# Kernel tuning notes

Measured on AMD Instinct MI355X. Metric: run time of the kernel, lower is better.

The kernel has to match this reference:

```python
import jax, jax.numpy as jnp
import numpy as np

B, T, D, H, E = 32, 512, 768, 12, 6  # batch, seq(=input_size), n_embd, num_heads, per-head dim
DFF = 4 * D
EPS = 1e-5


def setup_inputs() -> dict:
    key = jax.random.key(0)
    ks = jax.random.split(key, 10)
    s = 0.02
    return {
        "x": jax.random.normal(ks[0], (B, T, D), jnp.float32),
        "Wq": jax.random.normal(ks[1], (H, D, E), jnp.float32) * s,
        "Wk": jax.random.normal(ks[2], (H, D, E), jnp.float32) * s,
        "Wv": jax.random.normal(ks[3], (H, D, E), jnp.float32) * s,
        "Wo": jax.random.normal(ks[4], (H * E, D), jnp.float32) * s,
        "bo": jnp.zeros((D,), jnp.float32),
        "W1": jax.random.normal(ks[5], (D, DFF), jnp.float32) * s,
        "b1": jnp.zeros((DFF,), jnp.float32),
        "W2": jax.random.normal(ks[6], (DFF, D), jnp.float32) * s,
        "b2": jnp.zeros((D,), jnp.float32),
        "g1": jnp.ones((D,), jnp.float32),
        "beta1": jnp.zeros((D,), jnp.float32),
        "g2": jnp.ones((D,), jnp.float32),
        "beta2": jnp.zeros((D,), jnp.float32),
    }


def _layernorm(x, g, b):
    m = jnp.mean(x, axis=-1, keepdims=True)
    v = jnp.var(x, axis=-1, keepdims=True)  # biased, matches torch LayerNorm
    return (x - m) * jax.lax.rsqrt(v + EPS) * g + b


def reference(x, Wq, Wk, Wv, Wo, bo, W1, b1, W2, b2, g1, beta1, g2, beta2):
    # --- pre-LN multi-head causal attention (dropout = identity, eval mode) ---
    xn = _layernorm(x, g1, beta1)
    q = jnp.einsum("btd,hde->bhte", xn, Wq)
    k = jnp.einsum("btd,hde->bhte", xn, Wk)
    v = jnp.einsum("btd,hde->bhte", xn, Wv)
    scores = jnp.einsum("bhte,bhse->bhts", q, k) * (E ** -0.5)
    causal = jnp.tril(jnp.ones((T, T), dtype=bool))
    scores = jnp.where(causal, scores, -jnp.inf)
    w = jax.nn.softmax(scores, axis=-1)
    o = jnp.einsum("bhts,bhse->bhte", w, v)
    o = o.transpose(0, 2, 1, 3).reshape(B, T, H * E)  # concat heads -> [B,T,72]
    x = x + o @ Wo + bo
    # --- pre-LN feed-forward ---
    y = _layernorm(x, g2, beta2)
    ff = jax.nn.relu(y @ W1 + b1) @ W2 + b2
    return x + ff
```

## Files before the change

### kernel.cpp

```cpp
#include <hip/hip_runtime.h>
#include <hip/hip_bf16.h>

#define BT 16384
#define DIM 768
#define NH 12
#define DFF 3072

typedef __attribute__((ext_vector_type(8))) short short8;
typedef __attribute__((ext_vector_type(4))) float floatx4;
typedef __attribute__((ext_vector_type(4))) unsigned short ushort4b;

using bf16 = __hip_bfloat16;

static __device__ __forceinline__ float b2f(bf16 v) { return __bfloat162float(v); }
static __device__ __forceinline__ bf16 f2b(float v) { return __float2bfloat16(v); }
static __device__ __forceinline__ float blo(unsigned int u) { return __uint_as_float(u << 16); }
static __device__ __forceinline__ float bhi(unsigned int u) { return __uint_as_float(u & 0xffff0000u); }

static __device__ __forceinline__ void gload_lds16(const void* g, void* l) {
    __builtin_amdgcn_global_load_lds(
        (const __attribute__((address_space(1))) unsigned int*)g,
        (__attribute__((address_space(3))) unsigned int*)l, 16, 0, 0);
}

__global__ __launch_bounds__(256) void pack_small_kernel(
    const float* __restrict__ Wq, const float* __restrict__ Wk, const float* __restrict__ Wv,
    const float* __restrict__ Wo, bf16* __restrict__ wqkv, bf16* __restrict__ wo_t)
{
    int i = blockIdx.x * 256 + threadIdx.x;
    const int S0 = 256 * 768, S1 = 768 * 96;
    if (i < S0) {
        int c = i / 768, dd = i % 768;
        float v = 0.f;
        if (c < 216) {
            int sel = c / 72, cc = c % 72, h = cc / 6, e = cc % 6;
            const float* W = (sel == 0) ? Wq : (sel == 1) ? Wk : Wv;
            v = W[((size_t)h * 768 + dd) * 6 + e];
        }
        wqkv[i] = f2b(v);
    } else if ((i -= S0) < S1) {
        int n = i / 96, r = i % 96;
        wo_t[i] = f2b(r < 72 ? Wo[r * 768 + n] : 0.f);
    }
}

__global__ __launch_bounds__(256) void transpose_kernel(
    const float* __restrict__ in, bf16* __restrict__ out, int R, int C)
{
    __shared__ float t[32][33];
    int c0 = blockIdx.x * 32, r0 = blockIdx.y * 32;
    int cx = threadIdx.x & 31, ry = threadIdx.x >> 5;
#pragma unroll
    for (int j = 0; j < 4; j++)
        t[ry + j * 8][cx] = in[(size_t)(r0 + ry + j * 8) * C + c0 + cx];
    __syncthreads();
    int rx = cx, cy = ry;
#pragma unroll
    for (int j = 0; j < 4; j++)
        out[(size_t)(c0 + cy + j * 8) * R + r0 + rx] = f2b(t[rx][cy + j * 8]);
}

__global__ __launch_bounds__(192) void ln_kernel(
    const float* __restrict__ x, const float* __restrict__ g, const float* __restrict__ be,
    bf16* __restrict__ out)
{
    int row = blockIdx.x;
    int tid = threadIdx.x;
    const float4* xr = (const float4*)(x + (size_t)row * DIM);
    float4 v = xr[tid];
    float s = v.x + v.y + v.z + v.w;
    float s2 = v.x * v.x + v.y * v.y + v.z * v.z + v.w * v.w;
#pragma unroll
    for (int off = 32; off; off >>= 1) {
        s += __shfl_down(s, off);
        s2 += __shfl_down(s2, off);
    }
    __shared__ float red[6];
    int wv = tid >> 6, ln = tid & 63;
    if (ln == 0) { red[wv] = s; red[3 + wv] = s2; }
    __syncthreads();
    float ts = red[0] + red[1] + red[2];
    float ts2 = red[3] + red[4] + red[5];
    float mean = ts * (1.f / 768.f);
    float var = ts2 * (1.f / 768.f) - mean * mean;
    float rstd = rsqrtf(var + 1e-5f);
    int c = tid * 4;
    float o0 = (v.x - mean) * rstd * g[c + 0] + be[c + 0];
    float o1 = (v.y - mean) * rstd * g[c + 1] + be[c + 1];
    float o2 = (v.z - mean) * rstd * g[c + 2] + be[c + 2];
    float o3 = (v.w - mean) * rstd * g[c + 3] + be[c + 3];
    bf16 h0 = f2b(o0), h1 = f2b(o1), h2 = f2b(o2), h3 = f2b(o3);
    ushort4b pk;
    pk[0] = *(unsigned short*)&h0; pk[1] = *(unsigned short*)&h1;
    pk[2] = *(unsigned short*)&h2; pk[3] = *(unsigned short*)&h3;
    *(ushort4b*)(out + (size_t)row * DIM + c) = pk;
}

template <int NSLAB, bool RELU, bool BIAS, bool RES, bool BF16OUT>
__global__ __launch_bounds__(256) void gemm_kernel(
    const bf16* __restrict__ A, const bf16* __restrict__ Bt,
    const float* __restrict__ bias, const float* __restrict__ res,
    void* __restrict__ Cv, int M, int N, int K)
{
    constexpr int SMEM_BYTES = BF16OUT ? (128 * 136 * 2) : (NSLAB * 2 * 128 * 32 * 2);
    __shared__ __align__(16) char smem[SMEM_BYTES];
    bf16* lA = (bf16*)smem;
    bf16* lB = lA + NSLAB * 128 * 32;

    const int tid = threadIdx.x;
    const int bm = blockIdx.x * 128;
    const int bn = blockIdx.y * 128;
    const int wave = tid >> 6, lane = tid & 63;
    const int wm = (wave >> 1) * 64, wn = (wave & 1) * 64;
    const int quad = lane >> 4, l16 = lane & 15;
    const int lrow = lane >> 2;
    const int lkc = (lane & 3) * 8;

    floatx4 acc[4][4] = {};

    for (int k0 = 0; k0 < K; k0 += NSLAB * 32) {
#pragma unroll
        for (int s = 0; s < NSLAB; s++) {
#pragma unroll
            for (int it = 0; it < 2; it++) {
                int r = wave * 32 + it * 16;
                gload_lds16(A + (size_t)(bm + r + lrow) * K + k0 + s * 32 + lkc,
                            lA + s * 4096 + r * 32);
                gload_lds16(Bt + (size_t)(bn + r + lrow) * K + k0 + s * 32 + lkc,
                            lB + s * 4096 + r * 32);
            }
        }
        __syncthreads();
#pragma unroll
        for (int s = 0; s < NSLAB; s++) {
            short8 af[4], bfr[4];
#pragma unroll
            for (int mt = 0; mt < 4; mt++)
                af[mt] = *(const short8*)(lA + s * 4096 + (wm + mt * 16 + l16) * 32 + quad * 8);
#pragma unroll
            for (int nt = 0; nt < 4; nt++)
                bfr[nt] = *(const short8*)(lB + s * 4096 + (wn + nt * 16 + l16) * 32 + quad * 8);
#pragma unroll
            for (int mt = 0; mt < 4; mt++)
#pragma unroll
                for (int nt = 0; nt < 4; nt++)
                    acc[mt][nt] = __builtin_amdgcn_mfma_f32_16x16x32_bf16(af[mt], bfr[nt], acc[mt][nt], 0, 0, 0);
        }
        __syncthreads();
    }

    if constexpr (BF16OUT) {
        bf16* ltile = (bf16*)smem;
#pragma unroll
        for (int mt = 0; mt < 4; mt++) {
#pragma unroll
            for (int nt = 0; nt < 4; nt++) {
                int tc = wn + nt * 16 + l16;
#pragma unroll
                for (int r = 0; r < 4; r++) {
                    int tr = wm + mt * 16 + quad * 4 + r;
                    float v0 = acc[mt][nt][r];
                    if constexpr (BIAS) v0 += bias[bn + tc];
                    if constexpr (RELU) v0 = fmaxf(v0, 0.f);
                    ltile[tr * 136 + tc] = f2b(v0);
                }
            }
        }
        __syncthreads();
        bf16* C = (bf16*)Cv;
        int rr0 = tid >> 4, col8 = (tid & 15) * 8;
        int gc = bn + col8;
#pragma unroll
        for (int p = 0; p < 8; p++) {
            int rr = p * 16 + rr0;
            if (gc < N)
                *(short8*)(C + (size_t)(bm + rr) * N + gc) =
                    *(const short8*)(ltile + rr * 136 + col8);
        }
    } else {
        float* C = (float*)Cv;
#pragma unroll
        for (int mt = 0; mt < 4; mt++) {
#pragma unroll
            for (int nt = 0; nt < 4; nt++) {
                int gc = bn + wn + nt * 16 + l16;
                if (gc < N) {
#pragma unroll
                    for (int r = 0; r < 4; r++) {
                        int gr = bm + wm + mt * 16 + quad * 4 + r;
                        float v0 = acc[mt][nt][r];
                        if constexpr (BIAS) v0 += bias[gc];
                        if constexpr (RES) v0 += res[(size_t)gr * N + gc];
                        if constexpr (RELU) v0 = fmaxf(v0, 0.f);
                        C[(size_t)gr * N + gc] = v0;
                    }
                }
            }
        }
    }
}

template <bool RELU, bool BIAS, bool RES, bool BF16OUT>
__global__ __launch_bounds__(512, 2) void gemm256_kernel(
    const bf16* __restrict__ A, const bf16* __restrict__ Bt,
    const float* __restrict__ bias, const float* __restrict__ res,
    void* __restrict__ Cv, int M, int N, int K)
{
    extern __shared__ __align__(16) char smem[];
    const int NT = K >> 6;
    const int k8 = blockIdx.x & 7, q = blockIdx.x >> 3;
    const int bm = (k8 * 8 + (q & 7)) << 8;
    const int bn = (q >> 3) << 8;

    const int tid = threadIdx.x;
    const int w = tid >> 6, lane = tid & 63;
    const int wm = w >> 2, wn = w & 3;
    const int l16 = lane & 15, quad = lane >> 4;

    const int rstg = (w >> 1) * 16 + (lane >> 2);
    const int cstg = (w & 1) * 32 + ((((lane & 3) * 8)) ^ ((lane & 32) ? 16 : 0));
    const bf16* aSrc = A + (size_t)(bm + rstg) * K + cstg;
    const bf16* bSrc = Bt + (size_t)(bn + rstg) * K + cstg;
    char* dstBase = smem + w * 1024;

    const int xr = (quad * 16) ^ ((l16 & 8) ? 32 : 0);
    const int aOff = wm * 16384 + l16 * 64 + xr;
    const int bOff = 32768 + wn * 8192 + l16 * 64 + xr;

#define STAGE(P, ISB, H, T) { \
    const bf16* _s = ((ISB) ? bSrc : aSrc) + ((size_t)((H) * 128) * K + (size_t)(T) * 64); \
    char* _d = dstBase + (P) * 65536 + (ISB) * 32768 + (H) * 16384; \
    gload_lds16(_s, _d); \
    gload_lds16(_s + (size_t)64 * K, _d + 8192); }

#define BARX() asm volatile("s_barrier" ::: "memory")
#define VMW(N_) asm volatile("s_waitcnt vmcnt(" #N_ ")" ::: "memory")

    floatx4 acc[8][4] = {};
    short8 a[4][2], b[2][2][2];

#define LDA(QM, CB) { _Pragma("unroll") for (int fm = 0; fm < 4; fm++) { \
    _Pragma("unroll") for (int s = 0; s < 2; s++) \
        a[fm][s] = *(const short8*)((CB) + aOff + (QM) * 8192 + fm * 2048 + s * 1024); } }
#define LDB(QN, CB) { _Pragma("unroll") for (int fn = 0; fn < 2; fn++) { \
    _Pragma("unroll") for (int s = 0; s < 2; s++) \
        b[QN][fn][s] = *(const short8*)((CB) + bOff + (QN) * 4096 + fn * 2048 + s * 1024); } }
#define MM(QM, QN) { __builtin_amdgcn_s_setprio(1); \
    _Pragma("unroll") for (int fm = 0; fm < 4; fm++) { \
    _Pragma("unroll") for (int fn = 0; fn < 2; fn++) { \
    _Pragma("unroll") for (int s = 0; s < 2; s++) \
        acc[(QM)*4+fm][(QN)*2+fn] = __builtin_amdgcn_mfma_f32_16x16x32_bf16( \
            a[fm][s], b[QN][fn][s], acc[(QM)*4+fm][(QN)*2+fn], 0, 0, 0); } } \
    __builtin_amdgcn_s_setprio(0); }

    STAGE(0, 1, 0, 0); STAGE(0, 1, 1, 0); STAGE(0, 0, 0, 0); STAGE(0, 0, 1, 0);
    STAGE(1, 1, 0, 1); STAGE(1, 1, 1, 1); STAGE(1, 0, 0, 1);
    VMW(6);
    BARX();

    for (int g = 0; g < NT; ++g) {
        const int p = g & 1, pn = p ^ 1;
        const char* cb = smem + p * 65536;
        LDA(0, cb); LDB(0, cb);
        if (g + 1 < NT) STAGE(pn, 0, 1, g + 1);
        BARX(); MM(0, 0); BARX();
        LDB(1, cb);
        BARX(); MM(0, 1); BARX();
        LDA(1, cb);
        if (g + 2 < NT) STAGE(p, 1, 0, g + 2);
        BARX(); MM(1, 0); BARX();
        if (g + 2 < NT) { STAGE(p, 1, 1, g + 2); STAGE(p, 0, 0, g + 2); }
        BARX(); MM(1, 1);
        if (g < NT - 2) { VMW(6); } else { VMW(0); }
        BARX();
    }

    if constexpr (BF16OUT) {
        bf16* lt = (bf16*)smem;
#pragma unroll
        for (int RF = 0; RF < 8; RF++) {
            const int row = wm * 128 + (RF >> 2) * 64 + (RF & 3) * 16 + quad * 4;
#pragma unroll
            for (int CF = 0; CF < 4; CF++) {
                const int col = wn * 64 + (CF >> 1) * 32 + (CF & 1) * 16 + l16;
                float bv = BIAS ? bias[bn + col] : 0.f;
#pragma unroll
                for (int rr = 0; rr < 4; rr++) {
                    float v = acc[RF][CF][rr] + bv;
                    if constexpr (RELU) v = fmaxf(v, 0.f);
                    lt[(row + rr) * 280 + col] = f2b(v);
                }
            }
        }
        asm volatile("s_waitcnt lgkmcnt(0)" ::: "memory");
        BARX();
        bf16* C = (bf16*)Cv;
#pragma unroll
        for (int it = 0; it < 16; it++) {
            int c = it * 512 + tid;
            int rr = c >> 5, c8 = (c & 31) * 8;
            *(short8*)(C + (size_t)(bm + rr) * N + bn + c8) =
                *(const short8*)(lt + rr * 280 + c8);
        }
    } else {
        float* C = (float*)Cv;
#pragma unroll
        for (int RF = 0; RF < 8; RF++) {
            const int gr = bm + wm * 128 + (RF >> 2) * 64 + (RF & 3) * 16 + quad * 4;
#pragma unroll
            for (int CF = 0; CF < 4; CF++) {
                const int gc = bn + wn * 64 + (CF >> 1) * 32 + (CF & 1) * 16 + l16;
                float bv = BIAS ? bias[gc] : 0.f;
#pragma unroll
                for (int rr = 0; rr < 4; rr++) {
                    float v = acc[RF][CF][rr] + bv;
                    if constexpr (RES) v += res[(size_t)(gr + rr) * N + gc];
                    if constexpr (RELU) v = fmaxf(v, 0.f);
                    C[(size_t)(gr + rr) * N + gc] = v;
                }
            }
        }
    }
#undef STAGE
#undef BARX
#undef VMW
#undef LDA
#undef LDB
#undef MM
}

template <int NTC, int TPB, bool RELU, bool BIAS, bool RES, bool BF16OUT>
__global__ __launch_bounds__(512, 2) void gemm192_kernel(
    const bf16* __restrict__ A, const bf16* __restrict__ Bt,
    const float* __restrict__ bias, const float* __restrict__ res,
    void* __restrict__ Cv, int N)
{
    constexpr int KC = NTC * 64;
    constexpr int NG = NTC * TPB;
    extern __shared__ __align__(16) char smem[];

    const int k8 = blockIdx.x & 7, q = blockIdx.x >> 3;
    const int sid = (q >> 3) * 64 + k8 * 8 + (q & 7);
    const int bm = (sid & 63) << 8;
    const int bnBase = (sid >> 6) * (TPB * 192);

    const int tid = threadIdx.x;
    const int w = tid >> 6, lane = tid & 63;
    const int wm = w >> 1, wn = w & 1;
    const int l16 = lane & 15, quad = lane >> 4;

    const int rstg = (w >> 1) * 16 + (lane >> 2);
    const int cstg = (w & 1) * 32 + (((lane & 3) * 8) ^ ((lane & 32) ? 16 : 0));
    const bf16* aSrc = A + (size_t)(bm + rstg) * KC + cstg;
    const bf16* bSrc = Bt + (size_t)(bnBase + rstg) * KC + cstg;
    const int stgoff = w * 1024;

    const int xr = (quad * 16) ^ ((l16 & 8) ? 32 : 0);
    const int aoff = wm * 8192 + l16 * 64 + xr;
    const int boff = 32768 + wn * 12288 + l16 * 64 + xr;

#define STG2(BO, ISB, CH) gload_lds16( \
        ((ISB) ? bS2 : aS2) + (size_t)(CH) * 64 * KC, \
        smem + (BO) + (ISB) * 32768 + (CH) * 8192 + stgoff)

#define BARX() asm volatile("s_barrier" ::: "memory")
#define VMW(N_) asm volatile("s_waitcnt vmcnt(" #N_ ")" ::: "memory")
#define LGW0() asm volatile("s_waitcnt lgkmcnt(0)" ::: "memory")

    floatx4 acc[4][6] = {};
    short8 a[2][2][2], b[2][3][2];

#define LDA(QM, CB) { _Pragma("unroll") for (int fm = 0; fm < 2; fm++) { \
    _Pragma("unroll") for (int s = 0; s < 2; s++) \
        a[QM][fm][s] = *(const short8*)((CB) + aoff + (QM) * 4096 + fm * 2048 + s * 1024); } }
#define LDB(QN, CB) { _Pragma("unroll") for (int fn = 0; fn < 3; fn++) { \
    _Pragma("unroll") for (int s = 0; s < 2; s++) \
        b[QN][fn][s] = *(const short8*)((CB) + boff + (QN) * 6144 + fn * 2048 + s * 1024); } }
#define MM(QM, QN) { __builtin_amdgcn_s_setprio(1); \
    _Pragma("unroll") for (int fm = 0; fm < 2; fm++) { \
    _Pragma("unroll") for (int fn = 0; fn < 3; fn++) { \
    _Pragma("unroll") for (int s = 0; s < 2; s++) \
        acc[(QM)*2+fm][(QN)*3+fn] = __builtin_amdgcn_mfma_f32_16x16x32_bf16( \
            a[QM][fm][s], b[(QN)][fn][s], acc[(QM)*2+fm][(QN)*3+fn], 0, 0, 0); } } \
    __builtin_amdgcn_s_setprio(0); }

    {
        const bf16* aS2 = aSrc;           const bf16* bS2 = bSrc;
#pragma unroll
        for (int c = 0; c < 4; c++) STG2(0, 0, c);
#pragma unroll
        for (int c = 0; c < 3; c++) STG2(0, 1, c);
        aS2 = aSrc + 64; bS2 = bSrc + 64;
#pragma unroll
        for (int c = 0; c < 4; c++) STG2(57344, 0, c);
#pragma unroll
        for (int c = 0; c < 3; c++) STG2(57344, 1, c);
    }
    VMW(7);
    BARX();
    LDA(0, smem); LDB(0, smem);

    for (int G = 0; G < NG; ++G) {
        const int bo = (G & 1) * 57344;
        const char* cb = smem + bo;
        const char* nb = smem + (bo ^ 57344);
        const int v = G + 2;
        const bf16* aS2 = aSrc;
        const bf16* bS2 = bSrc;
        if (v < NG) {
            const int t2 = v / NTC, g2 = v - t2 * NTC;
            aS2 = aSrc + (size_t)g2 * 64;
            bS2 = bSrc + (size_t)t2 * (192 * (size_t)KC) + (size_t)g2 * 64;
        }
        LDA(1, cb);
        MM(0, 0);
        BARX();
        LDB(1, cb);
        MM(1, 0);
        VMW(0);
        BARX();
        if (v < NG) { STG2(bo, 0, 0); STG2(bo, 0, 1); STG2(bo, 0, 2); STG2(bo, 0, 3); }
        if (G + 1 < NG) LDB(0, nb);
        MM(1, 1);
        BARX();
        if (v < NG) { STG2(bo, 1, 0); STG2(bo, 1, 1); STG2(bo, 1, 2); }
        MM(0, 1);
        if (G + 1 < NG) LDA(0, nb);
        BARX();
    }

    if constexpr (!BF16OUT) {
        float* C = (float*)Cv;
        const int bn = bnBase;
#pragma unroll
        for (int mf = 0; mf < 4; mf++) {
            const int gr = bm + wm * 64 + mf * 16 + quad * 4;
#pragma unroll
            for (int nf = 0; nf < 6; nf++) {
                const int gc = bn + wn * 96 + nf * 16 + l16;
                float bv = BIAS ? bias[gc] : 0.f;
#pragma unroll
                for (int r = 0; r < 4; r++) {
                    float v = acc[mf][nf][r] + bv;
                    if constexpr (RES) v += res[(size_t)(gr + r) * N + gc];
                    if constexpr (RELU) v = fmaxf(v, 0.f);
                    C[(size_t)(gr + r) * N + gc] = v;
                }
            }
        }
    }
#undef STG2
#undef BARX
#undef VMW
#undef LGW0
#undef LDA
#undef LDB
#undef MM
}

__global__ __launch_bounds__(256) void attn_kernel(const bf16* __restrict__ qkv, bf16* __restrict__ o_pad)
{
    int blk = blockIdx.x;
    int half = blk & 1;
    int bh = blk >> 1;
    int b = bh / NH, h = bh % NH;
    int wave = threadIdx.x >> 6, lane = threadIdx.x & 63;
    const int jmap0[4] = {0, 2, 5, 7}, jmap1[4] = {1, 3, 4, 6};
    int j = half ? jmap1[wave] : jmap0[wave];
    int t = j * 64 + lane;
    int smax = half ? 448 : 512;

    __shared__ uint4 ks8[512];
    __shared__ uint4 vs8[512];
    const bf16* base = qkv + (size_t)b * 512 * 216;
    for (int s = threadIdx.x; s < smax; s += 256) {
        const unsigned int* kp = (const unsigned int*)(base + s * 216 + 72 + h * 6);
        const unsigned int* vp = (const unsigned int*)(base + s * 216 + 144 + h * 6);
        ks8[s] = make_uint4(kp[0], kp[1], kp[2], 0u);
        vs8[s] = make_uint4(vp[0], vp[1], vp[2], 0u);
    }
    __syncthreads();

    const float kSc = 0.4082482904638630f * 1.4426950408889634f;
    const unsigned int* qp = (const unsigned int*)(base + t * 216 + h * 6);
    unsigned int q01 = qp[0], q23 = qp[1], q45 = qp[2];
    float q0 = blo(q01) * kSc, q1 = bhi(q01) * kSc;
    float q2 = blo(q23) * kSc, q3 = bhi(q23) * kSc;
    float q4 = blo(q45) * kSc, q5 = bhi(q45) * kSc;

    float l = 0.f;
    float o0 = 0, o1 = 0, o2 = 0, o3 = 0, o4 = 0, o5 = 0;
    for (int s = 0; s <= t; s++) {
        uint4 kk = ks8[s];
        float sc = q0 * blo(kk.x);
        sc = fmaf(q1, bhi(kk.x), sc);
        sc = fmaf(q2, blo(kk.y), sc);
        sc = fmaf(q3, bhi(kk.y), sc);
        sc = fmaf(q4, blo(kk.z), sc);
        sc = fmaf(q5, bhi(kk.z), sc);
        float p = exp2f(sc);
        l += p;
        uint4 vv = vs8[s];
        o0 = fmaf(p, blo(vv.x), o0);
        o1 = fmaf(p, bhi(vv.x), o1);
        o2 = fmaf(p, blo(vv.y), o2);
        o3 = fmaf(p, bhi(vv.y), o3);
        o4 = fmaf(p, blo(vv.z), o4);
        o5 = fmaf(p, bhi(vv.z), o5);
    }
    float inv = 1.f / l;
    bf16* orow = o_pad + (size_t)(b * 512 + t) * 96 + h * 6;
    orow[0] = f2b(o0 * inv);
    orow[1] = f2b(o1 * inv);
    orow[2] = f2b(o2 * inv);
    orow[3] = f2b(o3 * inv);
    orow[4] = f2b(o4 * inv);
    orow[5] = f2b(o5 * inv);
}

extern "C" void kernel_launch(void* const* d_in, const int* in_sizes, int n_in,
                              void* d_out, int out_size, void* d_ws, size_t ws_size,
                              hipStream_t stream)
{
    const float* x   = (const float*)d_in[0];
    const float* Wq  = (const float*)d_in[1];
    const float* Wk  = (const float*)d_in[2];
    const float* Wv  = (const float*)d_in[3];
    const float* Wo  = (const float*)d_in[4];
    const float* bo  = (const float*)d_in[5];
    const float* W1  = (const float*)d_in[6];
    const float* b1  = (const float*)d_in[7];
    const float* W2  = (const float*)d_in[8];
    const float* b2  = (const float*)d_in[9];
    const float* g1  = (const float*)d_in[10];
    const float* be1 = (const float*)d_in[11];
    const float* g2  = (const float*)d_in[12];
    const float* be2 = (const float*)d_in[13];

    char* ws = (char*)d_ws;
    size_t off = 0;
    auto alloc = [&](size_t bytes) {
        void* p = ws + off;
        off = (off + bytes + 255) & ~(size_t)255;
        return p;
    };
    bf16*  xn    = (bf16*)alloc((size_t)BT * DIM * 2);
    bf16*  qkvb  = (bf16*)alloc((size_t)BT * 216 * 2);
    bf16*  o_pad = (bf16*)alloc((size_t)BT * 96 * 2);
    float* x1    = (float*)alloc((size_t)BT * DIM * 4);
    bf16*  ffb   = (bf16*)alloc((size_t)BT * DFF * 2);
    bf16*  wqkv  = (bf16*)alloc((size_t)256 * 768 * 2);
    bf16*  wo_t  = (bf16*)alloc((size_t)768 * 96 * 2);
    bf16*  w1t   = (bf16*)alloc((size_t)3072 * 768 * 2);
    bf16*  w2t   = (bf16*)alloc((size_t)768 * 3072 * 2);

    hipFuncSetAttribute(reinterpret_cast<const void*>(&gemm256_kernel<true, true, false, true>),
                        hipFuncAttributeMaxDynamicSharedMemorySize, 256 * 280 * 2);
    hipFuncSetAttribute(reinterpret_cast<const void*>(&gemm192_kernel<48, 1, false, true, true, false>),
                        hipFuncAttributeMaxDynamicSharedMemorySize, 114688);

    const int PACK_N = 256 * 768 + 768 * 96;
    pack_small_kernel<<<(PACK_N + 255) / 256, 256, 0, stream>>>(Wq, Wk, Wv, Wo, wqkv, wo_t);
    transpose_kernel<<<dim3(3072 / 32, 768 / 32), 256, 0, stream>>>(W1, w1t, 768, 3072);
    transpose_kernel<<<dim3(768 / 32, 3072 / 32), 256, 0, stream>>>(W2, w2t, 3072, 768);

    ln_kernel<<<BT, 192, 0, stream>>>(x, g1, be1, xn);
    gemm_kernel<2, false, false, false, true><<<dim3(128, 2), 256, 0, stream>>>(
        xn, wqkv, nullptr, nullptr, qkvb, BT, 216, 768);
    attn_kernel<<<32 * NH * 2, 256, 0, stream>>>(qkvb, o_pad);
    gemm_kernel<1, false, true, true, false><<<dim3(128, 6), 256, 0, stream>>>(
        o_pad, wo_t, bo, x, x1, BT, 768, 96);
    ln_kernel<<<BT, 192, 0, stream>>>(x1, g2, be2, xn);
    gemm256_kernel<true, true, false, true><<<768, 512, 256 * 280 * 2, stream>>>(
        xn, w1t, b1, nullptr, ffb, BT, 3072, 768);
    gemm192_kernel<48, 1, false, true, true, false><<<256, 512, 114688, stream>>>(
        ffb, w2t, b2, x1, (float*)d_out, 768);
}
```

Before: 416.5 us.

## Fuse output projection with second LayerNorm and merge weight prep kernels

Replaces the Wo projection GEMM and the separate LN2 kernel with one kernel that computes the 96-wide projection via MFMA, adds bias and residual, and reduces row statistics across waves in LDS. It then writes normalized bf16 rows through an LDS staging buffer. This drops one full fp32 read of x1 and a launch. The three weight-prep launches are also merged into a single 3D-grid kernel. The tradeoff is one block per 64 rows with about 100KB of LDS, giving only 256 blocks and low occupancy, and a single-pass variance formula.

```diff
diff --git a/kernel.cpp b/kernel.cpp
--- a/kernel.cpp
+++ b/kernel.cpp
@@ -23,32 +23,38 @@
         (__attribute__((address_space(3))) unsigned int*)l, 16, 0, 0);
 }
 
-__global__ __launch_bounds__(256) void pack_small_kernel(
+__global__ __launch_bounds__(256) void prep_kernel(
     const float* __restrict__ Wq, const float* __restrict__ Wk, const float* __restrict__ Wv,
-    const float* __restrict__ Wo, bf16* __restrict__ wqkv, bf16* __restrict__ wo_t)
-{
-    int i = blockIdx.x * 256 + threadIdx.x;
-    const int S0 = 256 * 768, S1 = 768 * 96;
-    if (i < S0) {
-        int c = i / 768, dd = i % 768;
-        float v = 0.f;
-        if (c < 216) {
-            int sel = c / 72, cc = c % 72, h = cc / 6, e = cc % 6;
-            const float* W = (sel == 0) ? Wq : (sel == 1) ? Wk : Wv;
-            v = W[((size_t)h * 768 + dd) * 6 + e];
-        }
-        wqkv[i] = f2b(v);
-    } else if ((i -= S0) < S1) {
-        int n = i / 96, r = i % 96;
-        wo_t[i] = f2b(r < 72 ? Wo[r * 768 + n] : 0.f);
-    }
-}
-
-__global__ __launch_bounds__(256) void transpose_kernel(
-    const float* __restrict__ in, bf16* __restrict__ out, int R, int C)
-{
+    const float* __restrict__ Wo, const float* __restrict__ W1, const float* __restrict__ W2,
+    bf16* __restrict__ wqkv, bf16* __restrict__ wo_t,
+    bf16* __restrict__ w1t, bf16* __restrict__ w2t)
+{
+    const int z = blockIdx.z;
+    if (z == 2) {
+        int i = (blockIdx.y * 96 + blockIdx.x) * 256 + threadIdx.x;
+        const int S0 = 256 * 768, S1 = 768 * 96;
+        if (i < S0) {
+            int c = i / 768, dd = i % 768;
+            float v = 0.f;
+            if (c < 216) {
+                int sel = c / 72, cc = c % 72, h = cc / 6, e = cc % 6;
+                const float* W = (sel == 0) ? Wq : (sel == 1) ? Wk : Wv;
+                v = W[((size_t)h * 768 + dd) * 6 + e];
+            }
+            wqkv[i] = f2b(v);
+        } else if ((i -= S0) < S1) {
+            int n = i / 96, r = i % 96;
+            wo_t[i] = f2b(r < 72 ? Wo[r * 768 + n] : 0.f);
+        }
+        return;
+    }
+    const float* in = z ? W2 : W1;
+    bf16* out = z ? w2t : w1t;
+    const int R = z ? 3072 : 768, C = z ? 768 : 3072;
+    const int bx = z ? blockIdx.y : blockIdx.x;
+    const int by = z ? blockIdx.x : blockIdx.y;
     __shared__ float t[32][33];
-    int c0 = blockIdx.x * 32, r0 = blockIdx.y * 32;
+    int c0 = bx * 32, r0 = by * 32;
     int cx = threadIdx.x & 31, ry = threadIdx.x >> 5;
 #pragma unroll
     for (int j = 0; j < 4; j++)
@@ -200,6 +206,119 @@
     }
 }
 
+__global__ __launch_bounds__(512) void proj_ln_kernel(
+    const bf16* __restrict__ o_pad, const bf16* __restrict__ wo_t,
+    const float* __restrict__ bo, const float* __restrict__ x,
+    const float* __restrict__ g, const float* __restrict__ be,
+    float* __restrict__ x1, bf16* __restrict__ xn)
+{
+    extern __shared__ __align__(16) char smem[];
+    bf16* pack = (bf16*)smem;
+    float* rsum = (float*)(smem + 100352);
+    float* rsq  = rsum + 256;
+    float* mlds = rsq + 256;
+    float* slds = mlds + 64;
+
+    const int bm = blockIdx.x * 64;
+    const int tid = threadIdx.x;
+    const int w = tid >> 6, lane = tid & 63;
+    const int wm = w >> 2, wn = w & 3;
+    const int l16 = lane & 15, quad = lane >> 4;
+
+    floatx4 acc[2][12] = {};
+    short8 a[2][3];
+#pragma unroll
+    for (int mf = 0; mf < 2; mf++)
+#pragma unroll
+        for (int ks = 0; ks < 3; ks++)
+            a[mf][ks] = *(const short8*)(o_pad +
+                (size_t)(bm + wm * 32 + mf * 16 + l16) * 96 + ks * 32 + quad * 8);
+#pragma unroll
+    for (int nf = 0; nf < 12; nf++) {
+        const int col = wn * 192 + nf * 16 + l16;
+#pragma unroll
+        for (int ks = 0; ks < 3; ks++) {
+            short8 bfr = *(const short8*)(wo_t + (size_t)col * 96 + ks * 32 + quad * 8);
+#pragma unroll
+            for (int mf = 0; mf < 2; mf++)
+                acc[mf][nf] = __builtin_amdgcn_mfma_f32_16x16x32_bf16(
+                    a[mf][ks], bfr, acc[mf][nf], 0, 0, 0);
+        }
+    }
+    float bov[12], gv[12], bev[12];
+#pragma unroll
+    for (int nf = 0; nf < 12; nf++) {
+        const int gc = wn * 192 + nf * 16 + l16;
+        bov[nf] = bo[gc]; gv[nf] = g[gc]; bev[nf] = be[gc];
+    }
+    float psum[2][4] = {}, psq[2][4] = {};
+#pragma unroll
+    for (int nf = 0; nf < 12; nf++) {
+        const int gc = wn * 192 + nf * 16 + l16;
+#pragma unroll
+        for (int mf = 0; mf < 2; mf++) {
+            const int gr = bm + wm * 32 + mf * 16 + quad * 4;
+#pragma unroll
+            for (int rr = 0; rr < 4; rr++) {
+                float v = acc[mf][nf][rr] + bov[nf] + x[(size_t)(gr + rr) * 768 + gc];
+                acc[mf][nf][rr] = v;
+                x1[(size_t)(gr + rr) * 768 + gc] = v;
+                psum[mf][rr] += v;
+                psq[mf][rr] = fmaf(v, v, psq[mf][rr]);
+            }
+        }
+    }
+#pragma unroll
+    for (int mf = 0; mf < 2; mf++)
+#pragma unroll
+        for (int rr = 0; rr < 4; rr++)
+#pragma unroll
+            for (int m = 1; m < 16; m <<= 1) {
+                psum[mf][rr] += __shfl_xor(psum[mf][rr], m);
+                psq[mf][rr]  += __shfl_xor(psq[mf][rr], m);
+            }
+    if (l16 == 0) {
+#pragma unroll
+        for (int mf = 0; mf < 2; mf++)
+#pragma unroll
+            for (int rr = 0; rr < 4; rr++) {
+                int row = wm * 32 + mf * 16 + quad * 4 + rr;
+                rsum[wn * 64 + row] = psum[mf][rr];
+                rsq [wn * 64 + row] = psq[mf][rr];
+            }
+    }
+    __syncthreads();
+    if (tid < 64) {
+        float s  = rsum[tid] + rsum[64 + tid] + rsum[128 + tid] + rsum[192 + tid];
+        float s2 = rsq [tid] + rsq [64 + tid] + rsq [128 + tid] + rsq [192 + tid];
+        float mean = s * (1.f / 768.f);
+        float var = s2 * (1.f / 768.f) - mean * mean;
+        mlds[tid] = mean;
+        slds[tid] = rsqrtf(var + 1e-5f);
+    }
+    __syncthreads();
+#pragma unroll
+    for (int mf = 0; mf < 2; mf++)
+#pragma unroll
+        for (int rr = 0; rr < 4; rr++) {
+            const int row = wm * 32 + mf * 16 + quad * 4 + rr;
+            const float mean = mlds[row], rstd = slds[row];
+#pragma unroll
+            for (int nf = 0; nf < 12; nf++) {
+                const int gc = wn * 192 + nf * 16 + l16;
+                float v = (acc[mf][nf][rr] - mean) * rstd * gv[nf] + bev[nf];
+                pack[row * 784 + gc] = f2b(v);
+            }
+        }
+    __syncthreads();
+#pragma unroll
+    for (int it = 0; it < 12; it++) {
+        int c = it * 512 + tid;
+        int rr = c / 96, cc = (c - rr * 96) * 8;
+        *(short8*)(xn + (size_t)(bm + rr) * 768 + cc) = *(const short8*)(pack + rr * 784 + cc);
+    }
+}
+
 template <bool RELU, bool BIAS, bool RES, bool BF16OUT>
 __global__ __launch_bounds__(512, 2) void gemm256_kernel(
     const bf16* __restrict__ A, const bf16* __restrict__ Bt,
@@ -365,7 +484,6 @@
 
 #define BARX() asm volatile("s_barrier" ::: "memory")
 #define VMW(N_) asm volatile("s_waitcnt vmcnt(" #N_ ")" ::: "memory")
-#define LGW0() asm volatile("s_waitcnt lgkmcnt(0)" ::: "memory")
 
     floatx4 acc[4][6] = {};
     short8 a[2][2][2], b[2][3][2];
@@ -452,7 +570,6 @@
 #undef STG2
 #undef BARX
 #undef VMW
-#undef LGW0
 #undef LDA
 #undef LDB
 #undef MM
@@ -558,19 +675,17 @@
                         hipFuncAttributeMaxDynamicSharedMemorySize, 256 * 280 * 2);
     hipFuncSetAttribute(reinterpret_cast<const void*>(&gemm192_kernel<48, 1, false, true, true, false>),
                         hipFuncAttributeMaxDynamicSharedMemorySize, 114688);
-
-    const int PACK_N = 256 * 768 + 768 * 96;
-    pack_small_kernel<<<(PACK_N + 255) / 256, 256, 0, stream>>>(Wq, Wk, Wv, Wo, wqkv, wo_t);
-    transpose_kernel<<<dim3(3072 / 32, 768 / 32), 256, 0, stream>>>(W1, w1t, 768, 3072);
-    transpose_kernel<<<dim3(768 / 32, 3072 / 32), 256, 0, stream>>>(W2, w2t, 3072, 768);
+    hipFuncSetAttribute(reinterpret_cast<const void*>(&proj_ln_kernel),
+                        hipFuncAttributeMaxDynamicSharedMemorySize, 103488);
+
+    prep_kernel<<<dim3(96, 24, 3), 256, 0, stream>>>(Wq, Wk, Wv, Wo, W1, W2,
+                                                     wqkv, wo_t, w1t, w2t);
 
     ln_kernel<<<BT, 192, 0, stream>>>(x, g1, be1, xn);
     gemm_kernel<2, false, false, false, true><<<dim3(128, 2), 256, 0, stream>>>(
         xn, wqkv, nullptr, nullptr, qkvb, BT, 216, 768);
     attn_kernel<<<32 * NH * 2, 256, 0, stream>>>(qkvb, o_pad);
-    gemm_kernel<1, false, true, true, false><<<dim3(128, 6), 256, 0, stream>>>(
-        o_pad, wo_t, bo, x, x1, BT, 768, 96);
-    ln_kernel<<<BT, 192, 0, stream>>>(x1, g2, be2, xn);
+    proj_ln_kernel<<<256, 512, 103488, stream>>>(o_pad, wo_t, bo, x, g2, be2, x1, xn);
     gemm256_kernel<true, true, false, true><<<768, 512, 256 * 280 * 2, stream>>>(
         xn, w1t, b1, nullptr, ffb, BT, 3072, 768);
     gemm192_kernel<48, 1, false, true, true, false><<<256, 512, 114688, stream>>>(
```

Result: faster. 404.2 us (-2.9%).
